# Performance work log

Measured on AMD Instinct MI355X. Metric: run time of the kernel, lower is better.

## Reference

```python
import jax, jax.numpy as jnp
import numpy as np

IN_F = 4096
OUT_F = 4096
RANK = 8
ALPHA = 8
SCALE = ALPHA / RANK


def setup_inputs() -> dict:
    key = jax.random.key(0)
    kx, kw, kb, ka = jax.random.split(key, 4)
    x = jax.random.normal(kx, (4, 4096, IN_F), dtype=jnp.float32)
    # base frozen linear params (torch Linear default init style, any values ok)
    W = jax.random.normal(kw, (OUT_F, IN_F), dtype=jnp.float32) * (1.0 / np.sqrt(IN_F))
    b = jax.random.normal(kb, (OUT_F,), dtype=jnp.float32) * 0.01
    # lora_A: kaiming_uniform_(a=sqrt(5)) -> U(-bound, bound), bound = sqrt(6/((1+5)*in_f)) = 1/sqrt(in_f)
    bound = 1.0 / np.sqrt(IN_F)
    lora_A = jax.random.uniform(ka, (RANK, IN_F), dtype=jnp.float32, minval=-bound, maxval=bound)
    # lora_B initialized to zeros per module; use small random values so the LoRA path is exercised
    lora_B = jax.random.normal(jax.random.fold_in(key, 7), (OUT_F, RANK), dtype=jnp.float32) * 0.02
    return {"x": x, "W": W, "b": b, "lora_A": lora_A, "lora_B": lora_B}


def reference(x, W, b, lora_A, lora_B):
    # base: x @ W.T + b  [B,S,out_f]
    base = jnp.einsum("bsi,oi->bso", x, W) + b
    # low-rank path: (x @ A.T) @ B.T * scale
    xa = jnp.einsum("bsi,ri->bsr", x, lora_A)  # [B,S,r]
    lora = jnp.einsum("bsr,or->bso", xa, lora_B)
    return base + lora * SCALE
```

## Files before the change

### kernel.cpp

```cpp
#include <hip/hip_runtime.h>
#include <cstdint>

#define K_IN   4096
#define N_OUT  4096
#define M_ROWS 16384
#define RANK   8
#define LSCALE 1.0f
#define NT     64
#define ROWB   8192
#define AHALF  1048576

typedef __attribute__((ext_vector_type(8))) short  short8;
typedef __attribute__((ext_vector_type(4))) float  floatx4;

__device__ __forceinline__ unsigned short f2bf(float f) {
  uint32_t u = __float_as_uint(f);
  u += 0x7FFFu + ((u >> 16) & 1u);
  return (unsigned short)(u >> 16);
}

__global__ __launch_bounds__(256) void fold_w_kernel(
    const float* __restrict__ W, const float* __restrict__ lA,
    const float* __restrict__ lB, unsigned short* __restrict__ Weff) {
  int idx = blockIdx.x * 256 + threadIdx.x;
  int o = idx >> 10;
  int k = (idx & 1023) << 2;
  float4 w = *reinterpret_cast<const float4*>(W + (size_t)o * K_IN + k);
#pragma unroll
  for (int r = 0; r < RANK; ++r) {
    float s = LSCALE * lB[o * RANK + r];
    float4 a = *reinterpret_cast<const float4*>(lA + r * K_IN + k);
    w.x += s * a.x; w.y += s * a.y; w.z += s * a.z; w.w += s * a.w;
  }
  ushort4 p;
  p.x = f2bf(w.x); p.y = f2bf(w.y); p.z = f2bf(w.z); p.w = f2bf(w.w);
  *reinterpret_cast<ushort4*>(Weff + (size_t)o * K_IN + k) = p;
}

__global__ __launch_bounds__(256) void cvt_x_kernel(
    const float* __restrict__ x, unsigned short* __restrict__ xb) {
  size_t i = ((size_t)blockIdx.x * 256 + threadIdx.x) * 8;
  float4 a = *reinterpret_cast<const float4*>(x + i);
  float4 c = *reinterpret_cast<const float4*>(x + i + 4);
  uint4 v;
  v.x = (uint32_t)f2bf(a.x) | ((uint32_t)f2bf(a.y) << 16);
  v.y = (uint32_t)f2bf(a.z) | ((uint32_t)f2bf(a.w) << 16);
  v.z = (uint32_t)f2bf(c.x) | ((uint32_t)f2bf(c.y) << 16);
  v.w = (uint32_t)f2bf(c.z) | ((uint32_t)f2bf(c.w) << 16);
  *reinterpret_cast<uint4*>(xb + i) = v;
}

__device__ __forceinline__ void gload_lds16(const void* g, void* l) {
  __builtin_amdgcn_global_load_lds(
      (const __attribute__((address_space(1))) void*)g,
      (__attribute__((address_space(3))) void*)l, 16, 0, 0);
}

#define BAR() do { asm volatile("" ::: "memory");                         \
    __builtin_amdgcn_s_barrier();                                         \
    asm volatile("" ::: "memory"); } while (0)

#define DSR(DST, ADDR, IMM)                                               \
  asm volatile("ds_read_b128 %0, %1 offset:%2"                            \
               : "=v"(DST) : "v"(ADDR), "i"(IMM))
#define WAIT_LDS() do {                                                   \
    asm volatile("s_waitcnt lgkmcnt(0)" ::: "memory");                    \
    __builtin_amdgcn_sched_barrier(0); } while (0)

__global__ __launch_bounds__(512, 2) void gemm256_kernel(
    const unsigned short* __restrict__ Xb, const unsigned short* __restrict__ Wb,
    const float* __restrict__ bias, float* __restrict__ out) {
  __shared__ alignas(16) char lds[2 * 65536];

  const int tid  = threadIdx.x;
  const int wave = tid >> 6, lane = tid & 63;
  const int wr = wave >> 2, wc = wave & 3;
  const int l15 = lane & 15, sq = lane >> 4;

  int bx  = blockIdx.x;
  int sbx = (bx & 7) * 128 + (bx >> 3);
  const int mt = sbx >> 4;
  const int nt = sbx & 15;

  const int rstg = tid >> 3;
  const int cbst = (((tid & 7) ^ ((tid >> 3) & 7)) << 4);
  const char* aBase = (const char*)Xb + (size_t)(mt * 256 + rstg) * ROWB + cbst;
  const char* bBase = (const char*)Wb + (size_t)(nt * 256 + rstg) * ROWB + cbst;

#define STAGE(H) do {                                                     \
    int th_ = (H) >> 2, hh_ = (H) & 3;                                    \
    const char* src_ = ((hh_ < 2) ? aBase + (size_t)hh_ * AHALF           \
                                  : bBase + (size_t)(hh_ - 2) * AHALF)    \
                       + th_ * 128;                                       \
    char* dst_ = lds + (th_ & 1) * 65536 + hh_ * 16384 + tid * 16;        \
    gload_lds16(src_, dst_);                                              \
    gload_lds16(src_ + (size_t)64 * ROWB, dst_ + 8192);                   \
  } while (0)

  const unsigned ldsb = (unsigned)(unsigned long long)
      (__attribute__((address_space(3))) char*)lds;
  const unsigned X = (unsigned)((l15 & 7) << 4);
  const unsigned aRow = ldsb + wr * 16384 + l15 * 128;
  const unsigned bRow = ldsb + (2 + (wc >> 1)) * 16384 + (wc & 1) * 8192
                        + l15 * 128;
  unsigned aCur0 = aRow + (((0u  + sq * 16) ) ^ X);
  unsigned aCur1 = aRow + (((64u + sq * 16) ) ^ X);
  unsigned bCur0 = bRow + (((0u  + sq * 16) ) ^ X);
  unsigned bCur1 = bRow + (((64u + sq * 16) ) ^ X);

#define LOAD_A(DST, MQ) do {                                              \
    _Pragma("unroll")                                                     \
    for (int fi = 0; fi < 4; ++fi)                                        \
      DSR(DST[fi],     aCur0, (MQ) * 8192 + fi * 2048);                   \
    _Pragma("unroll")                                                     \
    for (int fi = 0; fi < 4; ++fi)                                        \
      DSR(DST[4 + fi], aCur1, (MQ) * 8192 + fi * 2048);                   \
  } while (0)
#define LOAD_B(DST, NQ) do {                                              \
    _Pragma("unroll")                                                     \
    for (int fj = 0; fj < 2; ++fj)                                        \
      DSR(DST[fj],     bCur0, (NQ) * 4096 + fj * 2048);                   \
    _Pragma("unroll")                                                     \
    for (int fj = 0; fj < 2; ++fj)                                        \
      DSR(DST[2 + fj], bCur1, (NQ) * 4096 + fj * 2048);                   \
  } while (0)
#define MFMA_Q(MQ, NQ, AF, BF) do {                                       \
    __builtin_amdgcn_s_setprio(1);                                        \
    _Pragma("unroll")                                                     \
    for (int ks = 0; ks < 2; ++ks)                                        \
      _Pragma("unroll")                                                   \
      for (int fi = 0; fi < 4; ++fi)                                      \
        _Pragma("unroll")                                                 \
        for (int fj = 0; fj < 2; ++fj)                                    \
          acc[(MQ) * 4 + fi][(NQ) * 2 + fj] =                             \
              __builtin_amdgcn_mfma_f32_16x16x32_bf16(                    \
                  AF[ks * 4 + fi], BF[ks * 2 + fj],                       \
                  acc[(MQ) * 4 + fi][(NQ) * 2 + fj], 0, 0, 0);            \
    __builtin_amdgcn_s_setprio(0); } while (0)

  floatx4 acc[8][4];
#pragma unroll
  for (int i = 0; i < 8; ++i)
#pragma unroll
    for (int j = 0; j < 4; ++j)
      acc[i][j] = (floatx4){0.f, 0.f, 0.f, 0.f};

  for (int h = 0; h < 7; ++h) STAGE(h);
  asm volatile("s_waitcnt vmcnt(6)" ::: "memory");
  BAR();

  short8 afA[8], afB[8], bfC[4];

  for (int t = 0; t < NT; ++t) {
    const int p0 = 4 * t;

    LOAD_A(afA, 0);
    LOAD_B(bfC, 0);
    if (p0 + 7 < 4 * NT) STAGE(p0 + 7);
    BAR();
    WAIT_LDS();
    MFMA_Q(0, 0, afA, bfC);
    BAR();

    LOAD_A(afB, 1);
    if (p0 + 8 < 4 * NT) STAGE(p0 + 8);
    BAR();
    WAIT_LDS();
    MFMA_Q(1, 0, afB, bfC);
    BAR();

    LOAD_B(bfC, 1);
    if (p0 + 9 < 4 * NT) STAGE(p0 + 9);
    BAR();
    WAIT_LDS();
    MFMA_Q(1, 1, afB, bfC);
    BAR();

    if (p0 + 10 < 4 * NT) STAGE(p0 + 10);
    if (t <= NT - 3)      asm volatile("s_waitcnt vmcnt(6)" ::: "memory");
    else if (t == NT - 2) asm volatile("s_waitcnt vmcnt(0)" ::: "memory");
    BAR();
    MFMA_Q(0, 1, afA, bfC);
    BAR();

    aCur0 ^= 65536u; aCur1 ^= 65536u;
    bCur0 ^= 65536u; bCur1 ^= 65536u;
  }
#undef STAGE
#undef LOAD_A
#undef LOAD_B
#undef MFMA_Q

  const int row0 = mt * 256 + wr * 128 + sq * 4;
  const int col0 = nt * 256 + wc * 64 + l15;
#pragma unroll
  for (int j = 0; j < 4; ++j) {
    int col = col0 + j * 16;
    float bv = bias[col];
#pragma unroll
    for (int i = 0; i < 8; ++i) {
      int rowb = row0 + i * 16;
#pragma unroll
      for (int rr = 0; rr < 4; ++rr)
        out[(size_t)(rowb + rr) * N_OUT + col] = acc[i][j][rr] + bv;
    }
  }
}

__global__ __launch_bounds__(256) void fallback_kernel(
    const float* __restrict__ x, const float* __restrict__ W,
    const float* __restrict__ bias, const float* __restrict__ lA,
    const float* __restrict__ lB, float* __restrict__ out) {
  __shared__ float Xs[64][17];
  __shared__ float Ws[64][17];
  int tid = threadIdx.x;
  int tx = tid & 15, ty = tid >> 4;
  int bm = blockIdx.y * 64, bn = blockIdx.x * 64;
  float acc[4][4] = {};
  for (int k0 = 0; k0 < K_IN; k0 += 16) {
#pragma unroll
    for (int q = 0; q < 4; ++q) {
      int flat = q * 256 + tid;
      int r = flat >> 4, c = flat & 15;
      Xs[r][c] = x[(size_t)(bm + r) * K_IN + k0 + c];
      float w = W[(size_t)(bn + r) * K_IN + k0 + c];
#pragma unroll
      for (int rr = 0; rr < RANK; ++rr)
        w += LSCALE * lB[(bn + r) * RANK + rr] * lA[rr * K_IN + k0 + c];
      Ws[r][c] = w;
    }
    __syncthreads();
#pragma unroll
    for (int kk = 0; kk < 16; ++kk) {
      float av[4], bv[4];
#pragma unroll
      for (int i = 0; i < 4; ++i) av[i] = Xs[ty * 4 + i][kk];
#pragma unroll
      for (int j = 0; j < 4; ++j) bv[j] = Ws[tx * 4 + j][kk];
#pragma unroll
      for (int i = 0; i < 4; ++i)
#pragma unroll
        for (int j = 0; j < 4; ++j) acc[i][j] += av[i] * bv[j];
    }
    __syncthreads();
  }
#pragma unroll
  for (int i = 0; i < 4; ++i)
#pragma unroll
    for (int j = 0; j < 4; ++j)
      out[(size_t)(bm + ty * 4 + i) * N_OUT + bn + tx * 4 + j] =
          acc[i][j] + bias[bn + tx * 4 + j];
}

extern "C" void kernel_launch(void* const* d_in, const int* in_sizes, int n_in,
                              void* d_out, int out_size, void* d_ws, size_t ws_size,
                              hipStream_t stream) {
  const float* x  = (const float*)d_in[0];
  const float* W  = (const float*)d_in[1];
  const float* b  = (const float*)d_in[2];
  const float* lA = (const float*)d_in[3];
  const float* lB = (const float*)d_in[4];
  float* out = (float*)d_out;

  const size_t weff_bytes = (size_t)N_OUT * K_IN * 2;
  const size_t xb_bytes   = (size_t)M_ROWS * K_IN * 2;

  if (ws_size >= weff_bytes + xb_bytes) {
    unsigned short* Weff = (unsigned short*)d_ws;
    unsigned short* Xb   = (unsigned short*)((char*)d_ws + weff_bytes);
    fold_w_kernel<<<(int)(((size_t)N_OUT * K_IN / 4) / 256), 256, 0, stream>>>(W, lA, lB, Weff);
    cvt_x_kernel<<<(int)(((size_t)M_ROWS * K_IN / 8) / 256), 256, 0, stream>>>(x, Xb);
    gemm256_kernel<<<(M_ROWS / 256) * (N_OUT / 256), 512, 0, stream>>>(Xb, Weff, b, out);
  } else {
    dim3 grid(N_OUT / 64, M_ROWS / 64);
    fallback_kernel<<<grid, 256, 0, stream>>>(x, W, b, lA, lB, out);
  }
}
```

Before: 577.8 us.

## Restructure GEMM main loop with register double-buffered fragments and partial LDS waits

Rewrites the bf16 MFMA main loop so that LDS fragment reads for the next quarter, and for the next k-tile, are issued ahead of the MFMAs that consume earlier fragments. Full lgkmcnt(0) waits become graduated lgkmcnt(12/8/0) waits. A second B fragment buffer (bfD) is added, the number of barriers per iteration drops, and global-to-LDS staging is regrouped into one per-tile batch. The goal is to overlap LDS read latency with MFMA work and cut barrier stalls. The cost is extra registers under launch_bounds(512,2), plus new hazards in the staging and wait ordering that could break correctness or occupancy.

Result: no change. 583.6 us (+1.0%).

```diff
diff --git a/kernel.cpp b/kernel.cpp
--- a/kernel.cpp
+++ b/kernel.cpp
@@ -63,8 +63,8 @@
 #define DSR(DST, ADDR, IMM)                                               \
   asm volatile("ds_read_b128 %0, %1 offset:%2"                            \
                : "=v"(DST) : "v"(ADDR), "i"(IMM))
-#define WAIT_LDS() do {                                                   \
-    asm volatile("s_waitcnt lgkmcnt(0)" ::: "memory");                    \
+#define LGKM(N) do {                                                      \
+    asm volatile("s_waitcnt lgkmcnt(" #N ")" ::: "memory");               \
     __builtin_amdgcn_sched_barrier(0); } while (0)
 
 __global__ __launch_bounds__(512, 2) void gemm256_kernel(
@@ -87,12 +87,11 @@
   const char* aBase = (const char*)Xb + (size_t)(mt * 256 + rstg) * ROWB + cbst;
   const char* bBase = (const char*)Wb + (size_t)(nt * 256 + rstg) * ROWB + cbst;
 
-#define STAGE(H) do {                                                     \
-    int th_ = (H) >> 2, hh_ = (H) & 3;                                    \
-    const char* src_ = ((hh_ < 2) ? aBase + (size_t)hh_ * AHALF           \
-                                  : bBase + (size_t)(hh_ - 2) * AHALF)    \
-                       + th_ * 128;                                       \
-    char* dst_ = lds + (th_ & 1) * 65536 + hh_ * 16384 + tid * 16;        \
+#define STAGE_TH(TH, HH) do {                                             \
+    const char* src_ = ((HH) < 2 ? aBase + (size_t)(HH) * AHALF           \
+                                 : bBase + (size_t)((HH) - 2) * AHALF)    \
+                       + (TH) * 128;                                      \
+    char* dst_ = lds + ((TH) & 1) * 65536 + (HH) * 16384 + tid * 16;      \
     gload_lds16(src_, dst_);                                              \
     gload_lds16(src_ + (size_t)64 * ROWB, dst_ + 8192);                   \
   } while (0)
@@ -103,10 +102,10 @@
   const unsigned aRow = ldsb + wr * 16384 + l15 * 128;
   const unsigned bRow = ldsb + (2 + (wc >> 1)) * 16384 + (wc & 1) * 8192
                         + l15 * 128;
-  unsigned aCur0 = aRow + (((0u  + sq * 16) ) ^ X);
-  unsigned aCur1 = aRow + (((64u + sq * 16) ) ^ X);
-  unsigned bCur0 = bRow + (((0u  + sq * 16) ) ^ X);
-  unsigned bCur1 = bRow + (((64u + sq * 16) ) ^ X);
+  unsigned aCur0 = aRow + ((0u  + sq * 16) ^ X);
+  unsigned aCur1 = aRow + ((64u + sq * 16) ^ X);
+  unsigned bCur0 = bRow + ((0u  + sq * 16) ^ X);
+  unsigned bCur1 = bRow + ((64u + sq * 16) ^ X);
 
 #define LOAD_A(DST, MQ) do {                                              \
     _Pragma("unroll")                                                     \
@@ -145,48 +144,45 @@
     for (int j = 0; j < 4; ++j)
       acc[i][j] = (floatx4){0.f, 0.f, 0.f, 0.f};
 
-  for (int h = 0; h < 7; ++h) STAGE(h);
+  STAGE_TH(0, 0); STAGE_TH(0, 1); STAGE_TH(0, 2); STAGE_TH(0, 3);
+  STAGE_TH(1, 0); STAGE_TH(1, 1); STAGE_TH(1, 2);
   asm volatile("s_waitcnt vmcnt(6)" ::: "memory");
   BAR();
 
-  short8 afA[8], afB[8], bfC[4];
+  short8 afA[8], afB[8], bfC[4], bfD[4];
+  LOAD_A(afA, 0);
+  LOAD_B(bfC, 0);
 
   for (int t = 0; t < NT; ++t) {
-    const int p0 = 4 * t;
-
-    LOAD_A(afA, 0);
-    LOAD_B(bfC, 0);
-    if (p0 + 7 < 4 * NT) STAGE(p0 + 7);
-    BAR();
-    WAIT_LDS();
+    LOAD_B(bfD, 1);
+    LOAD_A(afB, 1);
+    if (t <= NT - 2) STAGE_TH(t + 1, 3);
+    LGKM(12);
     MFMA_Q(0, 0, afA, bfC);
     BAR();
 
-    LOAD_A(afB, 1);
-    if (p0 + 8 < 4 * NT) STAGE(p0 + 8);
-    BAR();
-    WAIT_LDS();
+    LGKM(8);
+    MFMA_Q(0, 1, afA, bfD);
+    BAR();
+
+    LGKM(0);
     MFMA_Q(1, 0, afB, bfC);
-    BAR();
-
-    LOAD_B(bfC, 1);
-    if (p0 + 9 < 4 * NT) STAGE(p0 + 9);
-    BAR();
-    WAIT_LDS();
-    MFMA_Q(1, 1, afB, bfC);
-    BAR();
-
-    if (p0 + 10 < 4 * NT) STAGE(p0 + 10);
-    if (t <= NT - 3)      asm volatile("s_waitcnt vmcnt(6)" ::: "memory");
-    else if (t == NT - 2) asm volatile("s_waitcnt vmcnt(0)" ::: "memory");
-    BAR();
-    MFMA_Q(0, 1, afA, bfC);
-    BAR();
-
-    aCur0 ^= 65536u; aCur1 ^= 65536u;
-    bCur0 ^= 65536u; bCur1 ^= 65536u;
-  }
-#undef STAGE
+    if (t <= NT - 2) asm volatile("s_waitcnt vmcnt(0)" ::: "memory");
+    BAR();
+
+    if (t <= NT - 2) {
+      aCur0 ^= 65536u; aCur1 ^= 65536u; bCur0 ^= 65536u; bCur1 ^= 65536u;
+      LOAD_A(afA, 0);
+      LOAD_B(bfC, 0);
+    }
+    if (t <= NT - 3) {
+      STAGE_TH(t + 2, 0); STAGE_TH(t + 2, 1); STAGE_TH(t + 2, 2);
+    }
+    __builtin_amdgcn_sched_barrier(0);
+    MFMA_Q(1, 1, afB, bfD);
+    BAR();
+  }
+#undef STAGE_TH
 #undef LOAD_A
 #undef LOAD_B
 #undef MFMA_Q
```
